# Kernel tuning notes

Hardware: AMD Instinct MI355X
Metric: run time of the kernel (lower is better)

## Reference

```python
import jax, jax.numpy as jnp
import numpy as np

L, D, H, V, T_BLK, B, T = 6, 768, 12, 32000, 1024, 4, 1024
HD = D // H          # head size = 64
FF = 4 * D           # FFN hidden
EPS = 1e-5


def _ln(x, g, b):
    m = x.mean(-1, keepdims=True)
    v = ((x - m) ** 2).mean(-1, keepdims=True)
    return (x - m) * jax.lax.rsqrt(v + EPS) * g + b


def _attn(q_in, kv_in, wqkv, wo, bo, causal):
    # wqkv: [3, D, D]; heads batched (equivalent to concat of per-head Linear outputs)
    Bq, Tq, _ = q_in.shape
    Tk = kv_in.shape[1]
    q = (q_in @ wqkv[0]).reshape(Bq, Tq, H, HD)
    k = (kv_in @ wqkv[1]).reshape(Bq, Tk, H, HD)
    v = (kv_in @ wqkv[2]).reshape(Bq, Tk, H, HD)
    wei = jnp.einsum('bqhd,bkhd->bhqk', q, k) * (HD ** -0.5)
    if causal:
        mask = jnp.tril(jnp.ones((Tq, Tk), dtype=bool))
        wei = jnp.where(mask, wei, -jnp.inf)
    wei = jax.nn.softmax(wei, axis=-1)
    out = jnp.einsum('bhqk,bkhd->bqhd', wei, v).reshape(Bq, Tq, D)
    return out @ wo + bo


def _ffn(x, w1, b1, w2, b2):
    return jax.nn.relu(x @ w1 + b1) @ w2 + b2


def _forward(idx, encoder_input,
             enc_tok, enc_pos, enc_qkv, enc_wo, enc_bo, enc_w1, enc_b1, enc_w2, enc_b2,
             enc_ln1g, enc_ln1b, enc_ln2g, enc_ln2b, enc_lnfg, enc_lnfb,
             dec_tok, dec_pos, dec_qkv, dec_wo, dec_bo, dec_cqkv, dec_cwo, dec_cbo,
             dec_w1, dec_b1, dec_w2, dec_b2,
             dec_ln1g, dec_ln1b, dec_ln2g, dec_ln2b, dec_ln3g, dec_ln3b,
             dec_lnfg, dec_lnfb, lm_w, lm_b):
    # ---- encoder (NOTE: original Head always applies causal tril, so encoder is causal) ----
    Te = encoder_input.shape[1]
    x = enc_tok[encoder_input] + enc_pos[:Te]
    for i in range(L):
        h = _ln(x, enc_ln1g[i], enc_ln1b[i])
        x = x + _attn(h, h, enc_qkv[i], enc_wo[i], enc_bo[i], causal=True)
        h = _ln(x, enc_ln2g[i], enc_ln2b[i])
        x = x + _ffn(h, enc_w1[i], enc_b1[i], enc_w2[i], enc_b2[i])
    enc_out = _ln(x, enc_lnfg, enc_lnfb)
    # ---- decoder ----
    Td = idx.shape[1]
    y = dec_tok[idx] + dec_pos[:Td]
    for i in range(L):
        h = _ln(y, dec_ln1g[i], dec_ln1b[i])
        y = y + _attn(h, h, dec_qkv[i], dec_wo[i], dec_bo[i], causal=True)
        h = _ln(y, dec_ln2g[i], dec_ln2b[i])
        y = y + _attn(h, enc_out, dec_cqkv[i], dec_cwo[i], dec_cbo[i], causal=False)
        h = _ln(y, dec_ln3g[i], dec_ln3b[i])
        y = y + _ffn(h, dec_w1[i], dec_b1[i], dec_w2[i], dec_b2[i])
    y = _ln(y, dec_lnfg, dec_lnfb)
    return y @ lm_w + lm_b  # logits [B, T, V]


def setup_inputs() -> dict:
    key = jax.random.key(0)
    keys = iter(jax.random.split(key, 80))
    def nrm(shape, s=0.02):
        return jax.random.normal(next(keys), shape, dtype=jnp.float32) * s
    z = lambda shape: jnp.zeros(shape, jnp.float32)
    o = lambda shape: jnp.ones(shape, jnp.float32)
    inp = {}
    inp['idx'] = jax.random.randint(next(keys), (B, T), 0, V)
    inp['encoder_input'] = jax.random.randint(next(keys), (B, T), 0, V)
    # encoder params
    inp['enc_tok'] = nrm((V, D)); inp['enc_pos'] = nrm((T_BLK, D))
    inp['enc_qkv'] = nrm((L, 3, D, D)); inp['enc_wo'] = nrm((L, D, D)); inp['enc_bo'] = z((L, D))
    inp['enc_w1'] = nrm((L, D, FF)); inp['enc_b1'] = z((L, FF))
    inp['enc_w2'] = nrm((L, FF, D)); inp['enc_b2'] = z((L, D))
    inp['enc_ln1g'] = o((L, D)); inp['enc_ln1b'] = z((L, D))
    inp['enc_ln2g'] = o((L, D)); inp['enc_ln2b'] = z((L, D))
    inp['enc_lnfg'] = o((D,)); inp['enc_lnfb'] = z((D,))
    # decoder params
    inp['dec_tok'] = nrm((V, D)); inp['dec_pos'] = nrm((T_BLK, D))
    inp['dec_qkv'] = nrm((L, 3, D, D)); inp['dec_wo'] = nrm((L, D, D)); inp['dec_bo'] = z((L, D))
    inp['dec_cqkv'] = nrm((L, 3, D, D)); inp['dec_cwo'] = nrm((L, D, D)); inp['dec_cbo'] = z((L, D))
    inp['dec_w1'] = nrm((L, D, FF)); inp['dec_b1'] = z((L, FF))
    inp['dec_w2'] = nrm((L, FF, D)); inp['dec_b2'] = z((L, D))
    inp['dec_ln1g'] = o((L, D)); inp['dec_ln1b'] = z((L, D))
    inp['dec_ln2g'] = o((L, D)); inp['dec_ln2b'] = z((L, D))
    inp['dec_ln3g'] = o((L, D)); inp['dec_ln3b'] = z((L, D))
    inp['dec_lnfg'] = o((D,)); inp['dec_lnfb'] = z((D,))
    inp['lm_w'] = nrm((D, V)); inp['lm_b'] = z((V,))
    return inp


def reference(idx, encoder_input,
              enc_tok, enc_pos, enc_qkv, enc_wo, enc_bo, enc_w1, enc_b1, enc_w2, enc_b2,
              enc_ln1g, enc_ln1b, enc_ln2g, enc_ln2b, enc_lnfg, enc_lnfb,
              dec_tok, dec_pos, dec_qkv, dec_wo, dec_bo, dec_cqkv, dec_cwo, dec_cbo,
              dec_w1, dec_b1, dec_w2, dec_b2,
              dec_ln1g, dec_ln1b, dec_ln2g, dec_ln2b, dec_ln3g, dec_ln3b,
              dec_lnfg, dec_lnfb, lm_w, lm_b):
    return _forward(idx, encoder_input,
                    enc_tok, enc_pos, enc_qkv, enc_wo, enc_bo, enc_w1, enc_b1, enc_w2, enc_b2,
                    enc_ln1g, enc_ln1b, enc_ln2g, enc_ln2b, enc_lnfg, enc_lnfb,
                    dec_tok, dec_pos, dec_qkv, dec_wo, dec_bo, dec_cqkv, dec_cwo, dec_cbo,
                    dec_w1, dec_b1, dec_w2, dec_b2,
                    dec_ln1g, dec_ln1b, dec_ln2g, dec_ln2b, dec_ln3g, dec_ln3b,
                    dec_lnfg, dec_lnfb, lm_w, lm_b)
```

## Files before the change

kernel.cpp:

```cpp
#include <hip/hip_runtime.h>


typedef __bf16 bf16x8 __attribute__((ext_vector_type(8)));
typedef float  f32x4  __attribute__((ext_vector_type(4)));
typedef unsigned short u16x4 __attribute__((ext_vector_type(4)));
typedef unsigned short u16x8 __attribute__((ext_vector_type(8)));

constexpr int Lc = 6, Dc = 768, Hc = 12, HDc = 64, Vc = 32000;
constexpr int Bc = 4, Tc = 1024, FFc = 3072;
constexpr int Mtot = Bc * Tc;

static __device__ __forceinline__ unsigned short f2bf(float f) {
  union { float f; unsigned u; } x; x.f = f;
  unsigned r = x.u + 0x7fffu + ((x.u >> 16) & 1u);
  return (unsigned short)(r >> 16);
}
static __device__ __forceinline__ float bf2f(unsigned short s) {
  union { unsigned u; float f; } c; c.u = (unsigned)s << 16; return c.f;
}

static __device__ __forceinline__ void gl_lds16(const unsigned short* g, unsigned short* l) {
  __builtin_amdgcn_global_load_lds(
      (const __attribute__((address_space(1))) unsigned int*)g,
      (__attribute__((address_space(3))) unsigned int*)l, 16, 0, 0);
}

template <int N> static __device__ __forceinline__ void wait_vm() {
  if constexpr (N == 0)      asm volatile("s_waitcnt vmcnt(0)" ::: "memory");
  else if constexpr (N == 2) asm volatile("s_waitcnt vmcnt(2)" ::: "memory");
  else if constexpr (N == 3) asm volatile("s_waitcnt vmcnt(3)" ::: "memory");
  else if constexpr (N == 4) asm volatile("s_waitcnt vmcnt(4)" ::: "memory");
}

static __device__ __forceinline__ float blockReduceSum(float v, float* red) {
  #pragma unroll
  for (int o = 32; o; o >>= 1) v += __shfl_xor(v, o, 64);
  int w = threadIdx.x >> 6;
  __syncthreads();
  if ((threadIdx.x & 63) == 0) red[w] = v;
  __syncthreads();
  return red[0] + red[1] + red[2] + red[3];
}

__global__ __launch_bounds__(256) void wconv_k(const float* __restrict__ W,
                                               unsigned short* __restrict__ WT,
                                               int K, int N) {
  __shared__ float t[32][33];
  const long zoff = (long)blockIdx.z * K * N;
  const int k0 = blockIdx.x * 32, n0 = blockIdx.y * 32;
  const int tid = threadIdx.x;
  const int rr = tid >> 3;
  const int cc = (tid & 7) * 4;
  f32x4 v = *reinterpret_cast<const f32x4*>(W + zoff + (long)(k0 + rr) * N + n0 + cc);
  #pragma unroll
  for (int j = 0; j < 4; j++) t[rr][cc + j] = v[j];
  __syncthreads();
  u16x4 o;
  #pragma unroll
  for (int j = 0; j < 4; j++) o[j] = f2bf(t[cc + j][rr]);
  *reinterpret_cast<u16x4*>(WT + zoff + (long)(n0 + rr) * K + k0 + cc) = o;
}

__global__ __launch_bounds__(256) void vtrans_k(const unsigned short* __restrict__ V,
                                                unsigned short* __restrict__ VT) {
  __shared__ unsigned short t[64][65];
  const int bh = blockIdx.y;
  const int b = bh / Hc, h = bh % Hc;
  const int t0 = blockIdx.x * 64;
  const int tid = threadIdx.x;
  const int rr = tid >> 3;
  const int c8 = (tid & 7) * 8;
  #pragma unroll
  for (int rep = 0; rep < 2; rep++) {
    int row = rep * 32 + rr;
    u16x8 v = *reinterpret_cast<const u16x8*>(V + (long)(b * Tc + t0 + row) * Dc + h * HDc + c8);
    #pragma unroll
    for (int j = 0; j < 8; j++) t[row][c8 + j] = v[j];
  }
  __syncthreads();
  #pragma unroll
  for (int rep = 0; rep < 2; rep++) {
    int hd = rep * 32 + rr;
    u16x8 o;
    #pragma unroll
    for (int j = 0; j < 8; j++) o[j] = t[c8 + j][hd];
    *reinterpret_cast<u16x8*>(VT + ((long)bh * HDc + hd) * Tc + t0 + c8) = o;
  }
}

__global__ __launch_bounds__(256) void embed_k(const int* __restrict__ idx,
                                               const float* __restrict__ tok,
                                               const float* __restrict__ pos,
                                               float* __restrict__ out) {
  const long row = blockIdx.x;
  const int t = (int)(row % Tc);
  const long id = idx[row];
  #pragma unroll
  for (int j = 0; j < 3; j++) {
    int e = threadIdx.x + j * 256;
    out[row * Dc + e] = tok[id * Dc + e] + pos[(long)t * Dc + e];
  }
}

__global__ __launch_bounds__(256) void ln_k(const float* __restrict__ X,
                                            const float* __restrict__ g,
                                            const float* __restrict__ bta,
                                            unsigned short* __restrict__ out) {
  __shared__ float red[4];
  const long row = blockIdx.x;
  const int tid = threadIdx.x;
  float v[3];
  #pragma unroll
  for (int j = 0; j < 3; j++) v[j] = X[row * Dc + tid + j * 256];
  float s = v[0] + v[1] + v[2];
  s = blockReduceSum(s, red);
  float mean = s * (1.f / 768.f);
  float q = 0.f;
  #pragma unroll
  for (int j = 0; j < 3; j++) { float d = v[j] - mean; q += d * d; }
  q = blockReduceSum(q, red);
  float rstd = rsqrtf(q * (1.f / 768.f) + 1e-5f);
  #pragma unroll
  for (int j = 0; j < 3; j++) {
    int e = tid + j * 256;
    out[row * Dc + e] = f2bf((v[j] - mean) * rstd * g[e] + bta[e]);
  }
}

template <bool CAUSAL>
__global__ __launch_bounds__(256) void flash_k(
    const unsigned short* __restrict__ Q,
    const unsigned short* __restrict__ K,
    const unsigned short* __restrict__ VT,
    unsigned short* __restrict__ O) {
  __shared__ __align__(16) unsigned short Ks[128 * 64];
  __shared__ __align__(16) unsigned short Vs[64 * 128];
  __shared__ __align__(16) unsigned short Ps[4][32 * 128];

  const int tid = threadIdx.x;
  const int lane = tid & 63;
  const int w = tid >> 6;
  const int lane16 = lane & 15;
  const int l4 = lane >> 4;
  const int bh = blockIdx.y;
  const int b = bh / Hc, h = bh % Hc;
  const int q0 = blockIdx.x * 128;

  const unsigned short* Qb = Q + ((long)b * Tc) * Dc + h * HDc;
  const unsigned short* Kb = K + ((long)b * Tc) * Dc + h * HDc;
  const unsigned short* Vb = VT + (long)bh * HDc * Tc;
  unsigned short* Ob = O + ((long)b * Tc) * Dc + h * HDc;

  bf16x8 qf[2][2];
  #pragma unroll
  for (int m = 0; m < 2; m++)
    #pragma unroll
    for (int kk = 0; kk < 2; kk++) {
      u16x8 raw = *reinterpret_cast<const u16x8*>(
          Qb + (long)(q0 + w * 32 + m * 16 + lane16) * Dc + kk * 32 + l4 * 8);
      bf16x8 f;
      #pragma unroll
      for (int j = 0; j < 8; j++) f[j] = (__bf16)(bf2f(raw[j]) * 0.125f);
      qf[m][kk] = f;
    }

  float mrow[2][4], lrow[2][4];
  f32x4 accO[2][4];
  #pragma unroll
  for (int m = 0; m < 2; m++)
    #pragma unroll
    for (int r = 0; r < 4; r++) { mrow[m][r] = -1e30f; lrow[m][r] = 0.f; }
  #pragma unroll
  for (int m = 0; m < 2; m++)
    #pragma unroll
    for (int d4 = 0; d4 < 4; d4++)
      #pragma unroll
      for (int r = 0; r < 4; r++) accO[m][d4][r] = 0.f;

  const int nch = CAUSAL ? (blockIdx.x + 1) : (Tc / 128);
  for (int c = 0; c < nch; c++) {
    const int k0 = c * 128;
    __syncthreads();
    #pragma unroll
    for (int it = 0; it < 4; it++) {
      int u = (it * 4 + w) * 64 + lane;
      int r = u >> 3, s = u & 7;
      gl_lds16(Kb + (long)(k0 + r) * Dc + ((s ^ (r & 7)) * 8), &Ks[(it * 4 + w) * 512]);
      int r2 = u >> 4, s2 = u & 15;
      gl_lds16(Vb + (long)r2 * Tc + k0 + ((s2 ^ (r2 & 7)) * 8), &Vs[(it * 4 + w) * 512]);
    }
    __syncthreads();

    f32x4 sacc[2][8];
    #pragma unroll
    for (int m = 0; m < 2; m++)
      #pragma unroll
      for (int n = 0; n < 8; n++)
        #pragma unroll
        for (int r = 0; r < 4; r++) sacc[m][n][r] = 0.f;
    #pragma unroll
    for (int n = 0; n < 8; n++) {
      int row = n * 16 + lane16;
      #pragma unroll
      for (int kk = 0; kk < 2; kk++) {
        bf16x8 kf = *reinterpret_cast<const bf16x8*>(
            &Ks[row * 64 + (((kk * 4 + l4) ^ (row & 7)) * 8)]);
        sacc[0][n] = __builtin_amdgcn_mfma_f32_16x16x32_bf16(qf[0][kk], kf, sacc[0][n], 0, 0, 0);
        sacc[1][n] = __builtin_amdgcn_mfma_f32_16x16x32_bf16(qf[1][kk], kf, sacc[1][n], 0, 0, 0);
      }
    }

    if (CAUSAL && c == nch - 1) {
      #pragma unroll
      for (int m = 0; m < 2; m++)
        #pragma unroll
        for (int n = 0; n < 8; n++)
          #pragma unroll
          for (int r = 0; r < 4; r++) {
            int kcol = k0 + n * 16 + lane16;
            int q = q0 + w * 32 + m * 16 + l4 * 4 + r;
            if (kcol > q) sacc[m][n][r] = -1e30f;
          }
    }

    #pragma unroll
    for (int m = 0; m < 2; m++)
      #pragma unroll
      for (int r = 0; r < 4; r++) {
        float smax = sacc[m][0][r];
        #pragma unroll
        for (int n = 1; n < 8; n++) smax = fmaxf(smax, sacc[m][n][r]);
        #pragma unroll
        for (int off = 1; off < 16; off <<= 1) smax = fmaxf(smax, __shfl_xor(smax, off, 64));
        float mold = mrow[m][r];
        float mnew = fmaxf(mold, smax);
        float sc = __expf(mold - mnew);
        float psum = 0.f;
        unsigned short pv[8];
        #pragma unroll
        for (int n = 0; n < 8; n++) {
          float p = __expf(sacc[m][n][r] - mnew);
          psum += p;
          pv[n] = f2bf(p);
        }
        #pragma unroll
        for (int off = 1; off < 16; off <<= 1) psum += __shfl_xor(psum, off, 64);
        lrow[m][r] = lrow[m][r] * sc + psum;
        mrow[m][r] = mnew;
        #pragma unroll
        for (int d4 = 0; d4 < 4; d4++) accO[m][d4][r] *= sc;
        int prow = m * 16 + l4 * 4 + r;
        #pragma unroll
        for (int n = 0; n < 8; n++) {
          int col = n * 16 + lane16;
          Ps[w][prow * 128 + (((col >> 3) ^ (prow & 7)) * 8) + (col & 7)] = pv[n];
        }
      }

    #pragma unroll
    for (int kk = 0; kk < 4; kk++) {
      bf16x8 pa[2];
      #pragma unroll
      for (int m = 0; m < 2; m++) {
        int arow = m * 16 + lane16;
        pa[m] = *reinterpret_cast<const bf16x8*>(
            &Ps[w][arow * 128 + (((kk * 4 + l4) ^ (arow & 7)) * 8)]);
      }
      #pragma unroll
      for (int d4 = 0; d4 < 4; d4++) {
        int vrow = d4 * 16 + lane16;
        bf16x8 vf = *reinterpret_cast<const bf16x8*>(
            &Vs[vrow * 128 + (((kk * 4 + l4) ^ (vrow & 7)) * 8)]);
        accO[0][d4] = __builtin_amdgcn_mfma_f32_16x16x32_bf16(pa[0], vf, accO[0][d4], 0, 0, 0);
        accO[1][d4] = __builtin_amdgcn_mfma_f32_16x16x32_bf16(pa[1], vf, accO[1][d4], 0, 0, 0);
      }
    }
  }

  #pragma unroll
  for (int m = 0; m < 2; m++)
    #pragma unroll
    for (int r = 0; r < 4; r++) {
      float inv = 1.f / lrow[m][r];
      int q = q0 + w * 32 + m * 16 + l4 * 4 + r;
      #pragma unroll
      for (int d4 = 0; d4 < 4; d4++)
        Ob[(long)q * Dc + d4 * 16 + lane16] = f2bf(accO[m][d4][r] * inv);
    }
}

template <int BM, int BN, int MF, int NF, int MINW,
          bool HASBIAS, bool RELU, bool HASRES, bool OUTBF, bool NT>
__global__ __launch_bounds__(256, MINW) void gemm_k(
    const unsigned short* __restrict__ A, long sAb, long sAh, int lda,
    const unsigned short* __restrict__ BT, long sBb, long sBh, int ldb,
    void* Cp, long sCb, long sCh, int ldc,
    const float* __restrict__ bias,
    const float* __restrict__ Res, int ldr,
    const unsigned short* __restrict__ A2,
    int K, int nH, float alpha) {
  constexpr int AI = BM / 64;
  constexpr int BI = BN / 64;
  constexpr int VC = AI + BI;
  __shared__ __align__(16) unsigned short As[2][BM * 32];
  __shared__ __align__(16) unsigned short Bs[2][BN * 32];

  const int tid = threadIdx.x;
  const int lane = tid & 63;
  const int w = tid >> 6;
  const int wr = w >> 1, wc = w & 1;
  const int lane16 = lane & 15;
  const int l4 = lane >> 4;

  const int z = blockIdx.z;
  const int bb = z / nH, hh = z % nH;
  const unsigned short* Abase = (A2 != nullptr && hh != 0) ? A2 : A;
  const long offA = sAb * bb + sAh * hh;
  const long offB = sBb * bb + sBh * hh;
  const long offC = sCb * bb + sCh * hh;

  const int gx = gridDim.x;
  const int nwg = gx * gridDim.y;
  const int id = blockIdx.y * gx + blockIdx.x;
  const int q8 = nwg >> 3, r8 = nwg & 7;
  const int xcd = id & 7, ord = id >> 3;
  const int swz = (xcd < r8 ? xcd * (q8 + 1) : r8 * (q8 + 1) + (xcd - r8) * q8) + ord;
  const int m0 = (swz % gx) * BM;
  const int n0 = (swz / gx) * BN;

  const int srow = lane >> 2;
  const int sslot = ((lane & 3) ^ ((srow >> 1) & 3)) * 8;

  const unsigned short* aP[AI];
  #pragma unroll
  for (int j = 0; j < AI; j++)
    aP[j] = Abase + offA + (long)(m0 + w * (BM / 4) + j * 16 + srow) * lda + sslot;
  const unsigned short* bP[BI];
  #pragma unroll
  for (int j = 0; j < BI; j++)
    bP[j] = BT + offB + (long)(n0 + w * (BN / 4) + j * 16 + srow) * ldb + sslot;

  f32x4 acc[MF][NF];
  #pragma unroll
  for (int m = 0; m < MF; m++)
    #pragma unroll
    for (int n = 0; n < NF; n++)
      #pragma unroll
      for (int r = 0; r < 4; r++) acc[m][n][r] = 0.f;

  auto STAGE = [&](int buf, int k0) {
    #pragma unroll
    for (int j = 0; j < AI; j++)
      gl_lds16(aP[j] + k0, &As[buf][(w * (BM / 4) + j * 16) * 32]);
    #pragma unroll
    for (int j = 0; j < BI; j++)
      gl_lds16(bP[j] + k0, &Bs[buf][(w * (BN / 4) + j * 16) * 32]);
  };

  const int nt = K / 32;
  STAGE(0, 0);
  int cur = 0;
  for (int t = 0; t < nt; t++) {
    if (t + 1 < nt) { STAGE(cur ^ 1, (t + 1) * 32); wait_vm<VC>(); }
    else            { wait_vm<0>(); }
    __builtin_amdgcn_sched_barrier(0);
    __builtin_amdgcn_s_barrier();
    __builtin_amdgcn_sched_barrier(0);

    bf16x8 afr[MF], bfr[NF];
    #pragma unroll
    for (int n = 0; n < NF; n++) {
      int row = wc * NF * 16 + n * 16 + lane16;
      bfr[n] = *reinterpret_cast<const bf16x8*>(
          &Bs[cur][row * 32 + ((l4 ^ ((row >> 1) & 3)) * 8)]);
    }
    #pragma unroll
    for (int m = 0; m < MF; m++) {
      int row = wr * MF * 16 + m * 16 + lane16;
      afr[m] = *reinterpret_cast<const bf16x8*>(
          &As[cur][row * 32 + ((l4 ^ ((row >> 1) & 3)) * 8)]);
    }
    __builtin_amdgcn_s_setprio(1);
    #pragma unroll
    for (int m = 0; m < MF; m++)
      #pragma unroll
      for (int n = 0; n < NF; n++)
        acc[m][n] = __builtin_amdgcn_mfma_f32_16x16x32_bf16(afr[m], bfr[n], acc[m][n], 0, 0, 0);
    __builtin_amdgcn_s_setprio(0);

    asm volatile("s_waitcnt lgkmcnt(0)" ::: "memory");
    __builtin_amdgcn_sched_barrier(0);
    __builtin_amdgcn_s_barrier();
    cur ^= 1;
  }

  const int r0 = m0 + wr * MF * 16;
  const int c0 = n0 + wc * NF * 16;
  #pragma unroll
  for (int m = 0; m < MF; m++) {
    #pragma unroll
    for (int n = 0; n < NF; n++) {
      #pragma unroll
      for (int r = 0; r < 4; r++) {
        int rr = r0 + m * 16 + l4 * 4 + r;
        int cc = c0 + n * 16 + lane16;
        float v = acc[m][n][r] * alpha;
        if constexpr (HASBIAS) v += bias[cc];
        if constexpr (RELU) v = fmaxf(v, 0.f);
        if constexpr (HASRES) v += Res[offC + (long)rr * ldr + cc];
        if constexpr (OUTBF) {
          ((unsigned short*)Cp)[offC + (long)rr * ldc + cc] = f2bf(v);
        } else {
          float* dst = (float*)Cp + offC + (long)rr * ldc + cc;
          if constexpr (NT) __builtin_nontemporal_store(v, dst);
          else              *dst = v;
        }
      }
    }
  }
}

extern "C" void kernel_launch(void* const* d_in, const int* in_sizes, int n_in,
                              void* d_out, int out_size, void* d_ws, size_t ws_size,
                              hipStream_t stream) {
  (void)in_sizes; (void)n_in; (void)out_size;

  const int*   idx      = (const int*)d_in[0];
  const int*   enc_in   = (const int*)d_in[1];
  const float* enc_tok  = (const float*)d_in[2];
  const float* enc_pos  = (const float*)d_in[3];
  const float* enc_qkv  = (const float*)d_in[4];
  const float* enc_wo   = (const float*)d_in[5];
  const float* enc_bo   = (const float*)d_in[6];
  const float* enc_w1   = (const float*)d_in[7];
  const float* enc_b1   = (const float*)d_in[8];
  const float* enc_w2   = (const float*)d_in[9];
  const float* enc_b2   = (const float*)d_in[10];
  const float* enc_ln1g = (const float*)d_in[11];
  const float* enc_ln1b = (const float*)d_in[12];
  const float* enc_ln2g = (const float*)d_in[13];
  const float* enc_ln2b = (const float*)d_in[14];
  const float* enc_lnfg = (const float*)d_in[15];
  const float* enc_lnfb = (const float*)d_in[16];
  const float* dec_tok  = (const float*)d_in[17];
  const float* dec_pos  = (const float*)d_in[18];
  const float* dec_qkv  = (const float*)d_in[19];
  const float* dec_wo   = (const float*)d_in[20];
  const float* dec_bo   = (const float*)d_in[21];
  const float* dec_cqkv = (const float*)d_in[22];
  const float* dec_cwo  = (const float*)d_in[23];
  const float* dec_cbo  = (const float*)d_in[24];
  const float* dec_w1   = (const float*)d_in[25];
  const float* dec_b1   = (const float*)d_in[26];
  const float* dec_w2   = (const float*)d_in[27];
  const float* dec_b2   = (const float*)d_in[28];
  const float* dec_ln1g = (const float*)d_in[29];
  const float* dec_ln1b = (const float*)d_in[30];
  const float* dec_ln2g = (const float*)d_in[31];
  const float* dec_ln2b = (const float*)d_in[32];
  const float* dec_ln3g = (const float*)d_in[33];
  const float* dec_ln3b = (const float*)d_in[34];
  const float* dec_lnfg = (const float*)d_in[35];
  const float* dec_lnfb = (const float*)d_in[36];
  const float* lm_w     = (const float*)d_in[37];
  const float* lm_b     = (const float*)d_in[38];

  constexpr long De2 = (long)Dc * Dc;
  constexpr long DF  = (long)Dc * FFc;

  unsigned short* wcache = (unsigned short*)d_out;
  size_t woff = 0;
  auto take = [&](size_t n) { unsigned short* p = wcache + woff; woff += n; return p; };
  unsigned short* enc_qkvT  = take(18ul * De2);
  unsigned short* enc_woT   = take(6ul * De2);
  unsigned short* enc_w1T   = take(6ul * DF);
  unsigned short* enc_w2T   = take(6ul * DF);
  unsigned short* dec_qkvT  = take(18ul * De2);
  unsigned short* dec_woT   = take(6ul * De2);
  unsigned short* dec_cqkvT = take(18ul * De2);
  unsigned short* dec_cwoT  = take(6ul * De2);
  unsigned short* dec_w1T   = take(6ul * DF);
  unsigned short* dec_w2T   = take(6ul * DF);

  char* ws = (char*)d_ws;
  const size_t need = (size_t)Dc * Vc * 2 + 2ull * Mtot * Dc * 4 + 3ull * Mtot * Dc * 2 +
                      3ull * Mtot * Dc * 2 + (size_t)Mtot * FFc * 2 + (size_t)Mtot * Dc * 2 +
                      (size_t)Bc * Hc * HDc * Tc * 2 + 4096;
  if (ws_size < need) return;
  auto takeW = [&](size_t bytes) { char* p = ws; ws += (bytes + 255) & ~255ull; return p; };
  unsigned short* lm_wT = (unsigned short*)takeW((size_t)Dc * Vc * 2);
  float* xe             = (float*)takeW((size_t)Mtot * Dc * 4);
  float* xd             = (float*)takeW((size_t)Mtot * Dc * 4);
  unsigned short* hbf   = (unsigned short*)takeW((size_t)Mtot * Dc * 2);
  unsigned short* qkvb  = (unsigned short*)takeW(3ull * Mtot * Dc * 2);
  unsigned short* ao    = (unsigned short*)takeW((size_t)Mtot * Dc * 2);
  unsigned short* mid   = (unsigned short*)takeW((size_t)Mtot * FFc * 2);
  unsigned short* eo    = (unsigned short*)takeW((size_t)Mtot * Dc * 2);
  unsigned short* vT    = (unsigned short*)takeW((size_t)Bc * Hc * HDc * Tc * 2);
  unsigned short* qb = qkvb;
  unsigned short* kb = qkvb + (size_t)Mtot * Dc;
  unsigned short* vb = qkvb + 2ull * Mtot * Dc;

  const dim3 TB(256);

  wconv_k<<<dim3(Dc/32, Dc/32, 18), TB, 0, stream>>>(enc_qkv, enc_qkvT, Dc, Dc);
  wconv_k<<<dim3(Dc/32, Dc/32,  6), TB, 0, stream>>>(enc_wo,  enc_woT,  Dc, Dc);
  wconv_k<<<dim3(Dc/32, FFc/32, 6), TB, 0, stream>>>(enc_w1,  enc_w1T,  Dc, FFc);
  wconv_k<<<dim3(FFc/32, Dc/32, 6), TB, 0, stream>>>(enc_w2,  enc_w2T,  FFc, Dc);
  wconv_k<<<dim3(Dc/32, Dc/32, 18), TB, 0, stream>>>(dec_qkv, dec_qkvT, Dc, Dc);
  wconv_k<<<dim3(Dc/32, Dc/32,  6), TB, 0, stream>>>(dec_wo,  dec_woT,  Dc, Dc);
  wconv_k<<<dim3(Dc/32, Dc/32, 18), TB, 0, stream>>>(dec_cqkv,dec_cqkvT,Dc, Dc);
  wconv_k<<<dim3(Dc/32, Dc/32,  6), TB, 0, stream>>>(dec_cwo, dec_cwoT, Dc, Dc);
  wconv_k<<<dim3(Dc/32, FFc/32, 6), TB, 0, stream>>>(dec_w1,  dec_w1T,  Dc, FFc);
  wconv_k<<<dim3(FFc/32, Dc/32, 6), TB, 0, stream>>>(dec_w2,  dec_w2T,  FFc, Dc);
  wconv_k<<<dim3(Dc/32, Vc/32,  1), TB, 0, stream>>>(lm_w,    lm_wT,    Dc, Vc);

  auto LN = [&](const float* X, const float* g, const float* b, unsigned short* o) {
    ln_k<<<dim3(Mtot), TB, 0, stream>>>(X, g, b, o);
  };
  auto QKV3 = [&](const unsigned short* Abf, const unsigned short* W3T) {
    gemm_k<128,64,4,2,4,false,false,false,true,false>
      <<<dim3(Mtot/128, Dc/64, 3), TB, 0, stream>>>(
        Abf, De2 * 0 + 0, 0, Dc, W3T, De2, 0, Dc,
        qkvb, (long)Mtot*Dc, 0, Dc, nullptr, nullptr, 0, nullptr, Dc, 1, 1.f);
  };
  auto CQKV = [&](const unsigned short* Abf, const unsigned short* WcT) {
    gemm_k<64,64,2,2,4,false,false,false,true,false>
      <<<dim3(Mtot/64, Dc/64, 3), TB, 0, stream>>>(
        Abf, 0, 0, Dc, WcT, 0, De2, Dc,
        qkvb, 0, (long)Mtot*Dc, Dc, nullptr, nullptr, 0, eo, Dc, 3, 1.f);
  };
  auto VT = [&]() {
    vtrans_k<<<dim3(Tc/64, Bc*Hc), TB, 0, stream>>>(vb, vT);
  };
  auto FLASH = [&](bool causal) {
    if (causal) flash_k<true ><<<dim3(Tc/128, Bc*Hc), TB, 0, stream>>>(qb, kb, vT, ao);
    else        flash_k<false><<<dim3(Tc/128, Bc*Hc), TB, 0, stream>>>(qb, kb, vT, ao);
  };
  auto ORES = [&](const unsigned short* Abf, const unsigned short* WT, const float* bias, float* X) {
    gemm_k<64,64,2,2,4,true,false,true,false,false>
      <<<dim3(Mtot/64, Dc/64, 1), TB, 0, stream>>>(
        Abf, 0, 0, Dc, WT, 0, 0, Dc,
        X, 0, 0, Dc, bias, X, Dc, nullptr, Dc, 1, 1.f);
  };
  auto FFN1 = [&](const unsigned short* Abf, const unsigned short* WT, const float* bias) {
    gemm_k<128,128,4,4,3,true,true,false,true,false>
      <<<dim3(Mtot/128, FFc/128, 1), TB, 0, stream>>>(
        Abf, 0, 0, Dc, WT, 0, 0, Dc,
        mid, 0, 0, FFc, bias, nullptr, 0, nullptr, Dc, 1, 1.f);
  };
  auto FFN2 = [&](const unsigned short* WT, const float* bias, float* X) {
    gemm_k<64,64,2,2,4,true,false,true,false,false>
      <<<dim3(Mtot/64, Dc/64, 1), TB, 0, stream>>>(
        mid, 0, 0, FFc, WT, 0, 0, FFc,
        X, 0, 0, Dc, bias, X, Dc, nullptr, FFc, 1, 1.f);
  };

  embed_k<<<dim3(Mtot), TB, 0, stream>>>(enc_in, enc_tok, enc_pos, xe);
  for (int i = 0; i < Lc; i++) {
    LN(xe, enc_ln1g + i * Dc, enc_ln1b + i * Dc, hbf);
    QKV3(hbf, enc_qkvT + (size_t)i * 3 * De2);
    VT(); FLASH(true);
    ORES(ao, enc_woT + (size_t)i * De2, enc_bo + i * Dc, xe);
    LN(xe, enc_ln2g + i * Dc, enc_ln2b + i * Dc, hbf);
    FFN1(hbf, enc_w1T + (size_t)i * DF, enc_b1 + i * FFc);
    FFN2(enc_w2T + (size_t)i * DF, enc_b2 + i * Dc, xe);
  }
  LN(xe, enc_lnfg, enc_lnfb, eo);

  embed_k<<<dim3(Mtot), TB, 0, stream>>>(idx, dec_tok, dec_pos, xd);
  for (int i = 0; i < Lc; i++) {
    LN(xd, dec_ln1g + i * Dc, dec_ln1b + i * Dc, hbf);
    QKV3(hbf, dec_qkvT + (size_t)i * 3 * De2);
    VT(); FLASH(true);
    ORES(ao, dec_woT + (size_t)i * De2, dec_bo + i * Dc, xd);
    LN(xd, dec_ln2g + i * Dc, dec_ln2b + i * Dc, hbf);
    CQKV(hbf, dec_cqkvT + (size_t)i * 3 * De2);
    VT(); FLASH(false);
    ORES(ao, dec_cwoT + (size_t)i * De2, dec_cbo + i * Dc, xd);
    LN(xd, dec_ln3g + i * Dc, dec_ln3b + i * Dc, hbf);
    FFN1(hbf, dec_w1T + (size_t)i * DF, dec_b1 + i * FFc);
    FFN2(dec_w2T + (size_t)i * DF, dec_b2 + i * Dc, xd);
  }
  LN(xd, dec_lnfg, dec_lnfb, hbf);

  gemm_k<128,128,4,4,3,true,false,false,false,true>
    <<<dim3(Mtot/128, Vc/128, 1), TB, 0, stream>>>(
      hbf, 0, 0, Dc, lm_wT, 0, 0, Dc,
      d_out, 0, 0, Vc, lm_b, nullptr, 0, nullptr, Dc, 1, 1.f);
}
```

Before: 3.990 ms.

## Fuse V transpose into flash attention, alias LDS, reverse causal tile order

Removes the separate V-transpose kernel and its scratch buffer. The flash kernel now loads V rows into registers and scatters them transposed into a swizzled LDS layout. LDS is pooled so the P buffers alias the K tile, which needs an extra barrier, and launch bounds request 3 blocks per CU. Causal blocks are scheduled heaviest-first, and the LM-head GEMM drops nontemporal stores and raises its occupancy hint. The scalar LDS scatter writes may add bank conflicts and instruction overhead inside the attention loop.

New measurement: 7.421 ms. 86.0% more time.

```diff
diff --git a/kernel.cpp b/kernel.cpp
--- a/kernel.cpp
+++ b/kernel.cpp
@@ -61,33 +61,6 @@
   *reinterpret_cast<u16x4*>(WT + zoff + (long)(n0 + rr) * K + k0 + cc) = o;
 }
 
-__global__ __launch_bounds__(256) void vtrans_k(const unsigned short* __restrict__ V,
-                                                unsigned short* __restrict__ VT) {
-  __shared__ unsigned short t[64][65];
-  const int bh = blockIdx.y;
-  const int b = bh / Hc, h = bh % Hc;
-  const int t0 = blockIdx.x * 64;
-  const int tid = threadIdx.x;
-  const int rr = tid >> 3;
-  const int c8 = (tid & 7) * 8;
-  #pragma unroll
-  for (int rep = 0; rep < 2; rep++) {
-    int row = rep * 32 + rr;
-    u16x8 v = *reinterpret_cast<const u16x8*>(V + (long)(b * Tc + t0 + row) * Dc + h * HDc + c8);
-    #pragma unroll
-    for (int j = 0; j < 8; j++) t[row][c8 + j] = v[j];
-  }
-  __syncthreads();
-  #pragma unroll
-  for (int rep = 0; rep < 2; rep++) {
-    int hd = rep * 32 + rr;
-    u16x8 o;
-    #pragma unroll
-    for (int j = 0; j < 8; j++) o[j] = t[c8 + j][hd];
-    *reinterpret_cast<u16x8*>(VT + ((long)bh * HDc + hd) * Tc + t0 + c8) = o;
-  }
-}
-
 __global__ __launch_bounds__(256) void embed_k(const int* __restrict__ idx,
                                                const float* __restrict__ tok,
                                                const float* __restrict__ pos,
@@ -128,14 +101,15 @@
 }
 
 template <bool CAUSAL>
-__global__ __launch_bounds__(256) void flash_k(
+__global__ __launch_bounds__(256, 3) void flash_k(
     const unsigned short* __restrict__ Q,
     const unsigned short* __restrict__ K,
-    const unsigned short* __restrict__ VT,
+    const unsigned short* __restrict__ V,
     unsigned short* __restrict__ O) {
-  __shared__ __align__(16) unsigned short Ks[128 * 64];
-  __shared__ __align__(16) unsigned short Vs[64 * 128];
-  __shared__ __align__(16) unsigned short Ps[4][32 * 128];
+  __shared__ __align__(16) unsigned short pool[24576];
+  unsigned short* Vs = pool;
+  unsigned short* Ks = pool + 8192;
+  unsigned short* Ps = pool + 8192;
 
   const int tid = threadIdx.x;
   const int lane = tid & 63;
@@ -144,11 +118,12 @@
   const int l4 = lane >> 4;
   const int bh = blockIdx.y;
   const int b = bh / Hc, h = bh % Hc;
-  const int q0 = blockIdx.x * 128;
+  const int qt = CAUSAL ? (int)(gridDim.x - 1 - blockIdx.x) : (int)blockIdx.x;
+  const int q0 = qt * 128;
 
   const unsigned short* Qb = Q + ((long)b * Tc) * Dc + h * HDc;
   const unsigned short* Kb = K + ((long)b * Tc) * Dc + h * HDc;
-  const unsigned short* Vb = VT + (long)bh * HDc * Tc;
+  const unsigned short* Vb = V + ((long)b * Tc) * Dc + h * HDc;
   unsigned short* Ob = O + ((long)b * Tc) * Dc + h * HDc;
 
   bf16x8 qf[2][2];
@@ -177,17 +152,33 @@
       #pragma unroll
       for (int r = 0; r < 4; r++) accO[m][d4][r] = 0.f;
 
-  const int nch = CAUSAL ? (blockIdx.x + 1) : (Tc / 128);
+  const int nch = CAUSAL ? (qt + 1) : (Tc / 128);
   for (int c = 0; c < nch; c++) {
     const int k0 = c * 128;
     __syncthreads();
+    u16x8 vr[4];
+    #pragma unroll
+    for (int rnd = 0; rnd < 4; rnd++) {
+      int row = rnd * 32 + (tid >> 3);
+      vr[rnd] = *reinterpret_cast<const u16x8*>(Vb + (long)(k0 + row) * Dc + (tid & 7) * 8);
+    }
     #pragma unroll
     for (int it = 0; it < 4; it++) {
       int u = (it * 4 + w) * 64 + lane;
       int r = u >> 3, s = u & 7;
       gl_lds16(Kb + (long)(k0 + r) * Dc + ((s ^ (r & 7)) * 8), &Ks[(it * 4 + w) * 512]);
-      int r2 = u >> 4, s2 = u & 15;
-      gl_lds16(Vb + (long)r2 * Tc + k0 + ((s2 ^ (r2 & 7)) * 8), &Vs[(it * 4 + w) * 512]);
+    }
+    #pragma unroll
+    for (int rnd = 0; rnd < 4; rnd++) {
+      int row = rnd * 32 + (tid >> 3);
+      int r8 = row >> 3, rlo = row & 7;
+      const unsigned short* vp = (const unsigned short*)&vr[rnd];
+      #pragma unroll
+      for (int j = 0; j < 8; j++) {
+        int d = (tid & 7) * 8 + j;
+        int key = ((d >> 3) ^ (d & 7)) & 7;
+        Vs[d * 128 + ((r8 ^ key) * 8) + rlo] = vp[j];
+      }
     }
     __syncthreads();
 
@@ -209,6 +200,7 @@
         sacc[1][n] = __builtin_amdgcn_mfma_f32_16x16x32_bf16(qf[1][kk], kf, sacc[1][n], 0, 0, 0);
       }
     }
+    __syncthreads();
 
     if (CAUSAL && c == nch - 1) {
       #pragma unroll
@@ -223,6 +215,7 @@
           }
     }
 
+    unsigned short* Pw = Ps + w * 4096;
     #pragma unroll
     for (int m = 0; m < 2; m++)
       #pragma unroll
@@ -253,7 +246,7 @@
         #pragma unroll
         for (int n = 0; n < 8; n++) {
           int col = n * 16 + lane16;
-          Ps[w][prow * 128 + (((col >> 3) ^ (prow & 7)) * 8) + (col & 7)] = pv[n];
+          Pw[prow * 128 + (((col >> 3) ^ (prow & 7)) * 8) + (col & 7)] = pv[n];
         }
       }
 
@@ -264,13 +257,14 @@
       for (int m = 0; m < 2; m++) {
         int arow = m * 16 + lane16;
         pa[m] = *reinterpret_cast<const bf16x8*>(
-            &Ps[w][arow * 128 + (((kk * 4 + l4) ^ (arow & 7)) * 8)]);
+            &Pw[arow * 128 + (((kk * 4 + l4) ^ (arow & 7)) * 8)]);
       }
       #pragma unroll
       for (int d4 = 0; d4 < 4; d4++) {
         int vrow = d4 * 16 + lane16;
+        int key = ((vrow >> 3) ^ (vrow & 7)) & 7;
         bf16x8 vf = *reinterpret_cast<const bf16x8*>(
-            &Vs[vrow * 128 + (((kk * 4 + l4) ^ (vrow & 7)) * 8)]);
+            &Vs[vrow * 128 + (((kk * 4 + l4) ^ key) * 8)]);
         accO[0][d4] = __builtin_amdgcn_mfma_f32_16x16x32_bf16(pa[0], vf, accO[0][d4], 0, 0, 0);
         accO[1][d4] = __builtin_amdgcn_mfma_f32_16x16x32_bf16(pa[1], vf, accO[1][d4], 0, 0, 0);
       }
@@ -290,7 +284,7 @@
 }
 
 template <int BM, int BN, int MF, int NF, int MINW,
-          bool HASBIAS, bool RELU, bool HASRES, bool OUTBF, bool NT>
+          bool HASBIAS, bool RELU, bool HASRES, bool OUTBF>
 __global__ __launch_bounds__(256, MINW) void gemm_k(
     const unsigned short* __restrict__ A, long sAb, long sAh, int lda,
     const unsigned short* __restrict__ BT, long sBb, long sBh, int ldb,
@@ -408,13 +402,8 @@
         if constexpr (HASBIAS) v += bias[cc];
         if constexpr (RELU) v = fmaxf(v, 0.f);
         if constexpr (HASRES) v += Res[offC + (long)rr * ldr + cc];
-        if constexpr (OUTBF) {
-          ((unsigned short*)Cp)[offC + (long)rr * ldc + cc] = f2bf(v);
-        } else {
-          float* dst = (float*)Cp + offC + (long)rr * ldc + cc;
-          if constexpr (NT) __builtin_nontemporal_store(v, dst);
-          else              *dst = v;
-        }
+        if constexpr (OUTBF) ((unsigned short*)Cp)[offC + (long)rr * ldc + cc] = f2bf(v);
+        else                 ((float*)Cp)[offC + (long)rr * ldc + cc] = v;
       }
     }
   }
@@ -484,8 +473,7 @@
 
   char* ws = (char*)d_ws;
   const size_t need = (size_t)Dc * Vc * 2 + 2ull * Mtot * Dc * 4 + 3ull * Mtot * Dc * 2 +
-                      3ull * Mtot * Dc * 2 + (size_t)Mtot * FFc * 2 + (size_t)Mtot * Dc * 2 +
-                      (size_t)Bc * Hc * HDc * Tc * 2 + 4096;
+                      3ull * Mtot * Dc * 2 + (size_t)Mtot * FFc * 2 + (size_t)Mtot * Dc * 2 + 4096;
   if (ws_size < need) return;
   auto takeW = [&](size_t bytes) { char* p = ws; ws += (bytes + 255) & ~255ull; return p; };
   unsigned short* lm_wT = (unsigned short*)takeW((size_t)Dc * Vc * 2);
@@ -496,7 +484,6 @@
   unsigned short* ao    = (unsigned short*)takeW((size_t)Mtot * Dc * 2);
   unsigned short* mid   = (unsigned short*)takeW((size_t)Mtot * FFc * 2);
   unsigned short* eo    = (unsigned short*)takeW((size_t)Mtot * Dc * 2);
-  unsigned short* vT    = (unsigned short*)takeW((size_t)Bc * Hc * HDc * Tc * 2);
   unsigned short* qb = qkvb;
   unsigned short* kb = qkvb + (size_t)Mtot * Dc;
   unsigned short* vb = qkvb + 2ull * Mtot * Dc;
@@ -519,38 +506,35 @@
     ln_k<<<dim3(Mtot), TB, 0, stream>>>(X, g, b, o);
   };
   auto QKV3 = [&](const unsigned short* Abf, const unsigned short* W3T) {
-    gemm_k<128,64,4,2,4,false,false,false,true,false>
+    gemm_k<128,64,4,2,4,false,false,false,true>
       <<<dim3(Mtot/128, Dc/64, 3), TB, 0, stream>>>(
-        Abf, De2 * 0 + 0, 0, Dc, W3T, De2, 0, Dc,
+        Abf, 0, 0, Dc, W3T, De2, 0, Dc,
         qkvb, (long)Mtot*Dc, 0, Dc, nullptr, nullptr, 0, nullptr, Dc, 1, 1.f);
   };
   auto CQKV = [&](const unsigned short* Abf, const unsigned short* WcT) {
-    gemm_k<64,64,2,2,4,false,false,false,true,false>
+    gemm_k<64,64,2,2,4,false,false,false,true>
       <<<dim3(Mtot/64, Dc/64, 3), TB, 0, stream>>>(
         Abf, 0, 0, Dc, WcT, 0, De2, Dc,
         qkvb, 0, (long)Mtot*Dc, Dc, nullptr, nullptr, 0, eo, Dc, 3, 1.f);
   };
-  auto VT = [&]() {
-    vtrans_k<<<dim3(Tc/64, Bc*Hc), TB, 0, stream>>>(vb, vT);
-  };
   auto FLASH = [&](bool causal) {
-    if (causal) flash_k<true ><<<dim3(Tc/128, Bc*Hc), TB, 0, stream>>>(qb, kb, vT, ao);
-    else        flash_k<false><<<dim3(Tc/128, Bc*Hc), TB, 0, stream>>>(qb, kb, vT, ao);
+    if (causal) flash_k<true ><<<dim3(Tc/128, Bc*Hc), TB, 0, stream>>>(qb, kb, vb, ao);
+    else        flash_k<false><<<dim3(Tc/128, Bc*Hc), TB, 0, stream>>>(qb, kb, vb, ao);
   };
   auto ORES = [&](const unsigned short* Abf, const unsigned short* WT, const float* bias, float* X) {
-    gemm_k<64,64,2,2,4,true,false,true,false,false>
+    gemm_k<64,64,2,2,4,true,false,true,false>
       <<<dim3(Mtot/64, Dc/64, 1), TB, 0, stream>>>(
         Abf, 0, 0, Dc, WT, 0, 0, Dc,
         X, 0, 0, Dc, bias, X, Dc, nullptr, Dc, 1, 1.f);
   };
   auto FFN1 = [&](const unsigned short* Abf, const unsigned short* WT, const float* bias) {
-    gemm_k<128,128,4,4,3,true,true,false,true,false>
+    gemm_k<128,128,4,4,3,true,true,false,true>
       <<<dim3(Mtot/128, FFc/128, 1), TB, 0, stream>>>(
         Abf, 0, 0, Dc, WT, 0, 0, Dc,
         mid, 0, 0, FFc, bias, nullptr, 0, nullptr, Dc, 1, 1.f);
   };
   auto FFN2 = [&](const unsigned short* WT, const float* bias, float* X) {
-    gemm_k<64,64,2,2,4,true,false,true,false,false>
+    gemm_k<64,64,2,2,4,true,false,true,false>
       <<<dim3(Mtot/64, Dc/64, 1), TB, 0, stream>>>(
         mid, 0, 0, FFc, WT, 0, 0, FFc,
         X, 0, 0, Dc, bias, X, Dc, nullptr, FFc, 1, 1.f);
@@ -560,7 +544,7 @@
   for (int i = 0; i < Lc; i++) {
     LN(xe, enc_ln1g + i * Dc, enc_ln1b + i * Dc, hbf);
     QKV3(hbf, enc_qkvT + (size_t)i * 3 * De2);
-    VT(); FLASH(true);
+    FLASH(true);
     ORES(ao, enc_woT + (size_t)i * De2, enc_bo + i * Dc, xe);
     LN(xe, enc_ln2g + i * Dc, enc_ln2b + i * Dc, hbf);
     FFN1(hbf, enc_w1T + (size_t)i * DF, enc_b1 + i * FFc);
@@ -572,11 +556,11 @@
   for (int i = 0; i < Lc; i++) {
     LN(xd, dec_ln1g + i * Dc, dec_ln1b + i * Dc, hbf);
     QKV3(hbf, dec_qkvT + (size_t)i * 3 * De2);
-    VT(); FLASH(true);
+    FLASH(true);
     ORES(ao, dec_woT + (size_t)i * De2, dec_bo + i * Dc, xd);
     LN(xd, dec_ln2g + i * Dc, dec_ln2b + i * Dc, hbf);
     CQKV(hbf, dec_cqkvT + (size_t)i * 3 * De2);
-    VT(); FLASH(false);
+    FLASH(false);
     ORES(ao, dec_cwoT + (size_t)i * De2, dec_cbo + i * Dc, xd);
     LN(xd, dec_ln3g + i * Dc, dec_ln3b + i * Dc, hbf);
     FFN1(hbf, dec_w1T + (size_t)i * DF, dec_b1 + i * FFc);
@@ -584,7 +568,7 @@
   }
   LN(xd, dec_lnfg, dec_lnfb, hbf);
 
-  gemm_k<128,128,4,4,3,true,false,false,false,true>
+  gemm_k<128,128,4,4,4,true,false,false,false>
     <<<dim3(Mtot/128, Vc/128, 1), TB, 0, stream>>>(
       hbf, 0, 0, Dc, lm_wT, 0, 0, Dc,
       d_out, 0, 0, Vc, lm_b, nullptr, 0, nullptr, Dc, 1, 1.f);
```
